# Performance work log

Hardware: AMD Instinct MI355X
Metric: run time of the kernel (lower is better)

The kernel has to match this reference:

```python
import jax, jax.numpy as jnp
import numpy as np


def setup_inputs() -> dict:
    key = jax.random.key(0)
    k1, k2, k3 = jax.random.split(key, 3)
    B, T, I, H, D = 32, 1024, 1024, 16, 64
    x = jax.random.normal(k1, (B, T, I), dtype=jnp.float32)
    kv_kernel = jax.random.normal(k2, (I, H, D, 2), dtype=jnp.float32) * (1.0 / np.sqrt(I))
    q_kernel = jax.random.normal(k3, (H, D), dtype=jnp.float32) * (1.0 / np.sqrt(D))
    return {"x": x, "kv_kernel": kv_kernel, "q_kernel": q_kernel}


def _attention_rnn(x, kv_kernel, q_kernel):
    # x: [B,T,I]; kv_kernel: [I,H,D,2]; q_kernel: [H,D]
    B, T, _ = x.shape
    H, D = q_kernel.shape
    # Projection + silu activation, done once for all timesteps (same math as per-step einsum)
    kv = jnp.einsum('bti,ihdk->bthdk', x, kv_kernel)
    kv = jax.nn.silu(kv)
    k = kv[..., 0]  # [B,T,H,D]
    v = kv[..., 1]  # [B,T,H,D]
    # Per-step attention score s_t = <q_h, k_th>
    s = jnp.einsum('hd,bthd->bth', q_kernel, k)  # [B,T,H]

    # Keras RNN zero-initialized states: num [B,H,D], den [B,H], max [B,H]
    init = (
        jnp.zeros((B, H, D), x.dtype),
        jnp.zeros((B, H), x.dtype),
        jnp.zeros((B, H), x.dtype),
    )

    def step(carry, inp):
        num, den, pmax = carry
        s_t, v_t = inp  # [B,H], [B,H,D]
        cmax = jnp.maximum(pmax, s_t)
        exp_max_diff = jnp.exp(pmax - cmax)
        sm = jnp.exp(s_t - cmax)
        den_n = sm + den * exp_max_diff
        num_n = v_t * sm[..., None] + num * exp_max_diff[..., None]
        h = num_n / den_n[..., None]          # [B,H,D]
        o = jnp.sum(h, axis=-2)               # concat_heads=False -> sum over heads: [B,D]
        return (num_n, den_n, cmax), o

    # scan over time (leading axis)
    _, outs = jax.lax.scan(step, init, (jnp.swapaxes(s, 0, 1), jnp.swapaxes(v, 0, 1)))
    return jnp.swapaxes(outs, 0, 1)  # [B,T,D]


def reference(x, kv_kernel, q_kernel):
    return _attention_rnn(x, kv_kernel, q_kernel)
```

## Files before the change

### kernel.cpp

```cpp
#include <hip/hip_runtime.h>
#include <hip/hip_bf16.h>

#define B_ 32
#define T_ 1024
#define H_ 16
#define D_ 64
#define M_ (B_*T_)
#define N_ (H_*D_*2)
#define K_ 1024
#define CHUNKS 32
#define CLEN (T_/CHUNKS)

typedef __bf16 bf16x8 __attribute__((ext_vector_type(8)));
typedef float  f32x4  __attribute__((ext_vector_type(4)));
typedef unsigned short u16x8 __attribute__((ext_vector_type(8)));

__device__ __forceinline__ float bf2f(unsigned short u){
  union{ float f; unsigned int i; } c; c.i = ((unsigned int)u) << 16; return c.f;
}
__device__ __forceinline__ unsigned short f2bf(float f){
  union{ float f; unsigned int i; } c; c.f = f;
  unsigned int r = (c.i + 0x7FFFu + ((c.i >> 16) & 1u)) >> 16;
  return (unsigned short)r;
}
__device__ __forceinline__ float silu(float x){ return x / (1.0f + __expf(-x)); }

__device__ __forceinline__ void gload16(const void* g, void* l){
  __builtin_amdgcn_global_load_lds(
      (const __attribute__((address_space(1))) void*)g,
      (__attribute__((address_space(3))) void*)l, 16, 0, 0);
}

#define BAR()   __builtin_amdgcn_s_barrier()
#define LGKM0() asm volatile("s_waitcnt lgkmcnt(0)" ::: "memory")
#define VM4()   asm volatile("s_waitcnt vmcnt(4)" ::: "memory")
#define VM0()   asm volatile("s_waitcnt vmcnt(0)" ::: "memory")

__global__ __launch_bounds__(256) void cvt_x(const float* __restrict__ x,
                                             unsigned short* __restrict__ xb, int n){
  int i = (blockIdx.x * 256 + threadIdx.x) * 8;
  int stride = gridDim.x * 256 * 8;
  for(; i < n; i += stride){
    float4 v0 = *(const float4*)(x + i);
    float4 v1 = *(const float4*)(x + i + 4);
    u16x8 o;
    o[0]=f2bf(v0.x); o[1]=f2bf(v0.y); o[2]=f2bf(v0.z); o[3]=f2bf(v0.w);
    o[4]=f2bf(v1.x); o[5]=f2bf(v1.y); o[6]=f2bf(v1.z); o[7]=f2bf(v1.w);
    *(u16x8*)(xb + i) = o;
  }
}

__global__ __launch_bounds__(256) void cvt_w(const float* __restrict__ w,
                                             unsigned short* __restrict__ wt){
  __shared__ unsigned short tile[64][65];
  int kt = blockIdx.x * 64, nt = blockIdx.y * 64;
  int t = threadIdx.x, tn = t & 63, tk4 = t >> 6;
  #pragma unroll
  for(int r = 0; r < 16; ++r){
    int kl = r * 4 + tk4;
    tile[tn][kl] = f2bf(w[(kt + kl) * N_ + nt + tn]);
  }
  __syncthreads();
  #pragma unroll
  for(int r = 0; r < 16; ++r){
    int nl = r * 4 + tk4;
    int n  = nt + nl;
    int np = (n & ~127) | ((n & 1) << 6) | ((n >> 1) & 63);
    wt[(size_t)np * K_ + kt + tn] = tile[nl][tn];
  }
}

__global__ __launch_bounds__(512, 2) void gemm8(
    const unsigned short* __restrict__ xb,
    const unsigned short* __restrict__ wt,
    const float*  __restrict__ q,
    unsigned short* __restrict__ vout,
    float* __restrict__ s)
{
  __shared__ __align__(16) char lds[131072];

  const int t = threadIdx.x, lane = t & 63, wid = t >> 6;
  const int wr = wid >> 2, wc = wid & 3;
  const int l15 = lane & 15, l4 = lane >> 4;

  const int id  = blockIdx.y * gridDim.x + blockIdx.x;
  const int swz = (id & 7) * 128 + (id >> 3);
  const int bx = swz & 127, by = swz >> 7;
  const int brow = bx * 256, bcol = by * 256;

  f32x4 acc[8][4] = {};
  bf16x8 af[8], b0[4], b1[4];

  const int swl   = l15 & 7;
  const int aoff0 = l15 * 128 + (((0 + l4) ^ swl) << 4);
  const int aoff1 = l15 * 128 + (((4 + l4) ^ swl) << 4);

  auto stage = [&](int buf, int op, int half, const unsigned short* src,
                   int rowbase, int kt){
    char* base = lds + buf * 65536 + op * 32768 + half * 16384;
    #pragma unroll
    for(int L = 0; L < 2; ++L){
      int idx = L * 512 + t;
      int r = idx >> 3, ss = idx & 7;
      gload16(src + (size_t)(rowbase + half * 128 + r) * K_
                  + kt * 64 + ((ss ^ (r & 7)) << 3),
              base + idx * 16);
    }
  };
  auto rdA = [&](int buf, int miBase){
    const char* base = lds + buf * 65536 + wr * 16384;
    #pragma unroll
    for(int m = 0; m < 4; ++m){
      af[m*2+0] = *(const bf16x8*)(base + (miBase + m) * 2048 + aoff0);
      af[m*2+1] = *(const bf16x8*)(base + (miBase + m) * 2048 + aoff1);
    }
  };
  auto rdB = [&](int buf, int niBase, bf16x8 (&dst)[4]){
    const char* base = lds + buf * 65536 + 32768 + (wc >> 1) * 16384 + (wc & 1) * 8192;
    #pragma unroll
    for(int n = 0; n < 2; ++n){
      dst[n*2+0] = *(const bf16x8*)(base + (niBase + n) * 2048 + aoff0);
      dst[n*2+1] = *(const bf16x8*)(base + (niBase + n) * 2048 + aoff1);
    }
  };
  auto mmaq = [&](int miBase, bf16x8 (&bb)[4], int niBase){
    __builtin_amdgcn_s_setprio(1);
    #pragma unroll
    for(int m = 0; m < 4; ++m)
      #pragma unroll
      for(int n = 0; n < 2; ++n)
        #pragma unroll
        for(int k = 0; k < 2; ++k)
          acc[miBase+m][niBase+n] = __builtin_amdgcn_mfma_f32_16x16x32_bf16(
              af[m*2+k], bb[n*2+k], acc[miBase+m][niBase+n], 0, 0, 0);
    __builtin_amdgcn_s_setprio(0);
  };

  stage(0,0,0, xb, brow, 0); stage(0,0,1, xb, brow, 0);
  stage(0,1,0, wt, bcol, 0); stage(0,1,1, wt, bcol, 0);
  stage(1,1,0, wt, bcol, 1); stage(1,1,1, wt, bcol, 1);
  VM4(); BAR();

  for(int i = 0; i < 7; ++i){
    const int t1 = 2*i + 1;
    const int t2 = 2*i + 2;
    const int t3 = 2*i + 3;
    rdA(0,0); rdB(0,0,b0); stage(1,0,0, xb, brow, t1);
    BAR(); LGKM0(); mmaq(0,b0,0); BAR();
    rdB(0,2,b1); stage(1,0,1, xb, brow, t1);
    BAR(); LGKM0(); mmaq(0,b1,2); BAR();
    rdA(0,4); stage(0,1,0, wt, bcol, t2);
    BAR(); LGKM0(); mmaq(4,b1,2); BAR();
    stage(0,1,1, wt, bcol, t2); VM4();
    BAR(); mmaq(4,b0,0); BAR();
    rdA(1,0); rdB(1,0,b0); stage(0,0,0, xb, brow, t2);
    BAR(); LGKM0(); mmaq(0,b0,0); BAR();
    rdB(1,2,b1); stage(0,0,1, xb, brow, t2);
    BAR(); LGKM0(); mmaq(0,b1,2); BAR();
    rdA(1,4); stage(1,1,0, wt, bcol, t3);
    BAR(); LGKM0(); mmaq(4,b1,2); BAR();
    stage(1,1,1, wt, bcol, t3); VM4();
    BAR(); mmaq(4,b0,0); BAR();
  }
  rdA(0,0); rdB(0,0,b0); stage(1,0,0, xb, brow, 15);
  BAR(); LGKM0(); mmaq(0,b0,0); BAR();
  rdB(0,2,b1); stage(1,0,1, xb, brow, 15);
  BAR(); LGKM0(); mmaq(0,b1,2); BAR();
  rdA(0,4);
  BAR(); LGKM0(); mmaq(4,b1,2); BAR();
  VM0();
  BAR(); mmaq(4,b0,0); BAR();
  rdA(1,0); rdB(1,0,b0);
  BAR(); LGKM0(); mmaq(0,b0,0); BAR();
  rdB(1,2,b1);
  BAR(); LGKM0(); mmaq(0,b1,2); BAR();
  rdA(1,4);
  BAR(); LGKM0(); mmaq(4,b1,2); BAR();
  mmaq(4,b0,0);

  const int hh = by * 2 + (wc >> 1);
  if(wc & 1){
    #pragma unroll
    for(int mi = 0; mi < 8; ++mi)
      #pragma unroll
      for(int r = 0; r < 4; ++r){
        const int gm = brow + wr*128 + mi*16 + l4*4 + r;
        const int bb = gm >> 10, tt = gm & (T_-1);
        unsigned short* vrow = vout + (((size_t)bb*H_ + hh)*T_ + tt)*D_;
        #pragma unroll
        for(int ni = 0; ni < 4; ++ni)
          vrow[ni*16 + l15] = f2bf(silu(acc[mi][ni][r]));
      }
  } else {
    float qv[4];
    #pragma unroll
    for(int ni = 0; ni < 4; ++ni) qv[ni] = q[hh*D_ + ni*16 + l15];
    #pragma unroll
    for(int mi = 0; mi < 8; ++mi)
      #pragma unroll
      for(int r = 0; r < 4; ++r){
        float sc = 0.f;
        #pragma unroll
        for(int ni = 0; ni < 4; ++ni) sc += qv[ni] * silu(acc[mi][ni][r]);
        sc += __shfl_xor(sc, 1); sc += __shfl_xor(sc, 2);
        sc += __shfl_xor(sc, 4); sc += __shfl_xor(sc, 8);
        if(l15 == 0){
          const int gm = brow + wr*128 + mi*16 + l4*4 + r;
          s[(size_t)gm * H_ + hh] = sc;
        }
      }
  }
}

__global__ __launch_bounds__(256) void scan1(
    const unsigned short* __restrict__ v, const float* __restrict__ s,
    float* __restrict__ snum, float* __restrict__ sden, float* __restrict__ smax)
{
  __shared__ float sst[CLEN*H_];
  const int blk = blockIdx.x;
  const int c = blk & (CHUNKS-1), b = blk >> 5;
  const int t = threadIdx.x, lane = t & 63, w = t >> 6, h0 = w * 4;

  const float* sbase = s + ((size_t)b*T_ + c*CLEN) * H_;
  for(int i = t; i < CLEN*H_; i += 256) sst[i] = sbase[i];
  __syncthreads();

  float m[4], den[4], num[4];
  #pragma unroll
  for(int j = 0; j < 4; ++j){ m[j] = -3.0e38f; den[j] = 0.f; num[j] = 0.f; }

  const unsigned short* vb = v + (((size_t)b*H_ + h0)*T_ + c*CLEN)*D_;
  for(int tt = 0; tt < CLEN; ++tt){
    #pragma unroll
    for(int j = 0; j < 4; ++j){
      float st = sst[tt*H_ + h0 + j];
      float vt = bf2f(vb[(size_t)j*T_*D_ + tt*D_ + lane]);
      float cm = fmaxf(m[j], st);
      float e  = __expf(m[j] - cm);
      float p  = __expf(st - cm);
      den[j] = den[j]*e + p;
      num[j] = num[j]*e + p*vt;
      m[j] = cm;
    }
  }
  #pragma unroll
  for(int j = 0; j < 4; ++j){
    int sb = (b*H_ + h0 + j)*CHUNKS + c;
    snum[(size_t)sb*64 + lane] = num[j];
    if(lane == 0){ sden[sb] = den[j]; smax[sb] = m[j]; }
  }
}

__global__ __launch_bounds__(256) void scan2h(
    const unsigned short* __restrict__ v, const float* __restrict__ s,
    const float* __restrict__ snum, const float* __restrict__ sden,
    const float* __restrict__ smax, float* __restrict__ out)
{
  __shared__ float sst[CLEN*H_];
  __shared__ float oacc[4][CLEN][76];
  const int blk = blockIdx.x;
  const int c = blk & (CHUNKS-1), b = blk >> 5;
  const int t = threadIdx.x, lane = t & 63, w = t >> 6, h0 = w * 4;

  const float* sbase = s + ((size_t)b*T_ + c*CLEN) * H_;
  for(int i = t; i < CLEN*H_; i += 256) sst[i] = sbase[i];
  __syncthreads();

  float num[4], den[4], m[4];
  #pragma unroll
  for(int j = 0; j < 4; ++j){ num[j] = 0.f; den[j] = 0.f; m[j] = -3.0e38f; }

  for(int cc = 0; cc < c; ++cc){
    #pragma unroll
    for(int j = 0; j < 4; ++j){
      int sb = (b*H_ + h0 + j)*CHUNKS + cc;
      float m2 = smax[sb], d2 = sden[sb], n2 = snum[(size_t)sb*64 + lane];
      float cm = fmaxf(m[j], m2);
      float e1 = __expf(m[j]-cm), e2 = __expf(m2-cm);
      den[j] = den[j]*e1 + d2*e2;
      num[j] = num[j]*e1 + n2*e2;
      m[j] = cm;
    }
  }

  const unsigned short* vb = v + (((size_t)b*H_ + h0)*T_ + c*CLEN)*D_;
  for(int tt = 0; tt < CLEN; ++tt){
    float o = 0.f;
    #pragma unroll
    for(int j = 0; j < 4; ++j){
      float st = sst[tt*H_ + h0 + j];
      float vt = bf2f(vb[(size_t)j*T_*D_ + tt*D_ + lane]);
      float cm = fmaxf(m[j], st);
      float e = __expf(m[j]-cm), p = __expf(st-cm);
      den[j] = den[j]*e + p;
      num[j] = num[j]*e + p*vt;
      m[j] = cm;
      o += num[j] / den[j];
    }
    oacc[w][tt][lane] = o;
  }
  __syncthreads();

  {
    int tt = t >> 3, db = (t & 7) * 8;
    float* ob = out + ((size_t)b*T_ + c*CLEN + tt) * D_ + db;
    #pragma unroll
    for(int qd = 0; qd < 2; ++qd){
      f32x4 a0 = *(const f32x4*)&oacc[0][tt][db + qd*4];
      f32x4 a1 = *(const f32x4*)&oacc[1][tt][db + qd*4];
      f32x4 a2 = *(const f32x4*)&oacc[2][tt][db + qd*4];
      f32x4 a3 = *(const f32x4*)&oacc[3][tt][db + qd*4];
      f32x4 r = (a0 + a1) + (a2 + a3);
      *(f32x4*)(ob + qd*4) = r;
    }
  }
}

extern "C" void kernel_launch(void* const* d_in, const int* in_sizes, int n_in,
                              void* d_out, int out_size, void* d_ws, size_t ws_size,
                              hipStream_t stream){
  (void)in_sizes; (void)n_in; (void)out_size; (void)ws_size;
  const float* x = (const float*)d_in[0];
  const float* w = (const float*)d_in[1];
  const float* q = (const float*)d_in[2];
  float* out = (float*)d_out;
  char* ws = (char*)d_ws;

  unsigned short* wt   = (unsigned short*)(ws);
  unsigned short* xb   = (unsigned short*)(ws + (4u  << 20));
  unsigned short* vbuf = (unsigned short*)(ws + (68u << 20));
  float* s    = (float*)(ws + (132u << 20));
  float* snum = (float*)(ws + (8u  << 20));
  float* sden = (float*)(ws + (12u << 20));
  float* smax = (float*)(ws + (12u << 20) + (1u << 16));

  cvt_x<<<2048, 256, 0, stream>>>(x, xb, M_ * K_);
  cvt_w<<<dim3(K_/64, N_/64), 256, 0, stream>>>(w, wt);
  gemm8<<<dim3(M_/256, N_/256), 512, 0, stream>>>(xb, wt, q, vbuf, s);
  scan1<<<B_*CHUNKS, 256, 0, stream>>>(vbuf, s, snum, sden, smax);
  scan2h<<<B_*CHUNKS, 256, 0, stream>>>(vbuf, s, snum, sden, smax, out);
}
```

Measured before the change: 259.6 us.

## Use lazy max rescaling in scan and halve the number of time chunks

The online-softmax recurrence now keeps the running max fixed unless a new score exceeds it by more than a threshold. Most steps then need one exp instead of two and no max update. The number of time chunks is halved, so each block scans longer sequences and the prefix combine is shorter, with the output-staging layout adjusted to match. This lowers arithmetic per step but cuts parallelism to half as many blocks, adds a divergent branch, and lets accumulators grow by up to e^8 relative to the stored max.

Result: slower. 390.0 us (+50.3%).

```diff
diff --git a/kernel.cpp b/kernel.cpp
--- a/kernel.cpp
+++ b/kernel.cpp
@@ -8,8 +8,9 @@
 #define M_ (B_*T_)
 #define N_ (H_*D_*2)
 #define K_ 1024
-#define CHUNKS 32
+#define CHUNKS 16
 #define CLEN (T_/CHUNKS)
+#define THR_ 8.0f
 
 typedef __bf16 bf16x8 __attribute__((ext_vector_type(8)));
 typedef float  f32x4  __attribute__((ext_vector_type(4)));
@@ -218,7 +219,7 @@
 {
   __shared__ float sst[CLEN*H_];
   const int blk = blockIdx.x;
-  const int c = blk & (CHUNKS-1), b = blk >> 5;
+  const int c = blk & (CHUNKS-1), b = blk / CHUNKS;
   const int t = threadIdx.x, lane = t & 63, w = t >> 6, h0 = w * 4;
 
   const float* sbase = s + ((size_t)b*T_ + c*CLEN) * H_;
@@ -235,12 +236,17 @@
     for(int j = 0; j < 4; ++j){
       float st = sst[tt*H_ + h0 + j];
       float vt = bf2f(vb[(size_t)j*T_*D_ + tt*D_ + lane]);
-      float cm = fmaxf(m[j], st);
-      float e  = __expf(m[j] - cm);
-      float p  = __expf(st - cm);
-      den[j] = den[j]*e + p;
-      num[j] = num[j]*e + p*vt;
-      m[j] = cm;
+      float d  = st - m[j];
+      if(d > THR_){
+        float e = __expf(-d);
+        den[j] = den[j]*e + 1.f;
+        num[j] = num[j]*e + vt;
+        m[j] = st;
+      } else {
+        float p = __expf(d);
+        den[j] += p;
+        num[j] += p*vt;
+      }
     }
   }
   #pragma unroll
@@ -257,9 +263,9 @@
     const float* __restrict__ smax, float* __restrict__ out)
 {
   __shared__ float sst[CLEN*H_];
-  __shared__ float oacc[4][CLEN][76];
+  __shared__ float oacc[4][CLEN][68];
   const int blk = blockIdx.x;
-  const int c = blk & (CHUNKS-1), b = blk >> 5;
+  const int c = blk & (CHUNKS-1), b = blk / CHUNKS;
   const int t = threadIdx.x, lane = t & 63, w = t >> 6, h0 = w * 4;
 
   const float* sbase = s + ((size_t)b*T_ + c*CLEN) * H_;
@@ -290,11 +296,17 @@
     for(int j = 0; j < 4; ++j){
       float st = sst[tt*H_ + h0 + j];
       float vt = bf2f(vb[(size_t)j*T_*D_ + tt*D_ + lane]);
-      float cm = fmaxf(m[j], st);
-      float e = __expf(m[j]-cm), p = __expf(st-cm);
-      den[j] = den[j]*e + p;
-      num[j] = num[j]*e + p*vt;
-      m[j] = cm;
+      float d  = st - m[j];
+      if(d > THR_){
+        float e = __expf(-d);
+        den[j] = den[j]*e + 1.f;
+        num[j] = num[j]*e + vt;
+        m[j] = st;
+      } else {
+        float p = __expf(d);
+        den[j] += p;
+        num[j] += p*vt;
+      }
       o += num[j] / den[j];
     }
     oacc[w][tt][lane] = o;
@@ -302,10 +314,10 @@
   __syncthreads();
 
   {
-    int tt = t >> 3, db = (t & 7) * 8;
+    int tt = t >> 2, db = (t & 3) * 16;
     float* ob = out + ((size_t)b*T_ + c*CLEN + tt) * D_ + db;
     #pragma unroll
-    for(int qd = 0; qd < 2; ++qd){
+    for(int qd = 0; qd < 4; ++qd){
       f32x4 a0 = *(const f32x4*)&oacc[0][tt][db + qd*4];
       f32x4 a1 = *(const f32x4*)&oacc[1][tt][db + qd*4];
       f32x4 a2 = *(const f32x4*)&oacc[2][tt][db + qd*4];
```
